# Kernel tuning notes

Hardware: AMD Instinct MI355X
Metric: run time of the kernel (lower is better)

The kernel has to match this reference:

```python
import jax, jax.numpy as jnp
import numpy as np

B, VD, SD, CD, H, HEADS = 16384, 2048, 1024, 512, 256, 4
DH = H // HEADS
EPS = 1e-5


def layer_norm(x, g, b):
    m = jnp.mean(x, axis=-1, keepdims=True)
    v = jnp.var(x, axis=-1, keepdims=True)
    return (x - m) * jax.lax.rsqrt(v + EPS) * g + b


def setup_inputs() -> dict:
    key = jax.random.key(0)
    ks = jax.random.split(key, 16)
    sc = 0.02
    inp = {
        'fv': jax.random.normal(ks[0], (B, VD), jnp.float32),
        'fs': jax.random.normal(ks[1], (B, SD), jnp.float32),
        'fc': jax.random.normal(ks[2], (B, CD), jnp.float32),
        # projection linears + layernorms
        'Wv': jax.random.normal(ks[3], (H, VD), jnp.float32) * sc,
        'bv': jnp.zeros((H,), jnp.float32),
        'gv': jnp.ones((H,), jnp.float32), 'bev': jnp.zeros((H,), jnp.float32),
        'Ws': jax.random.normal(ks[4], (H, SD), jnp.float32) * sc,
        'bs': jnp.zeros((H,), jnp.float32),
        'gs': jnp.ones((H,), jnp.float32), 'bes': jnp.zeros((H,), jnp.float32),
        'Wc': jax.random.normal(ks[5], (H, CD), jnp.float32) * sc,
        'bc': jnp.zeros((H,), jnp.float32),
        'gc_': jnp.ones((H,), jnp.float32), 'bec': jnp.zeros((H,), jnp.float32),
        # MultiheadAttention packed in-proj and out-proj
        'in_w': jax.random.normal(ks[6], (3 * H, H), jnp.float32) * sc,
        'in_b': jnp.zeros((3 * H,), jnp.float32),
        'out_w': jax.random.normal(ks[7], (H, H), jnp.float32) * sc,
        'out_b': jnp.zeros((H,), jnp.float32),
        # post-attention layernorm
        'gn': jnp.ones((H,), jnp.float32), 'gb': jnp.zeros((H,), jnp.float32),
        # gating MLP: Linear(3H,64) -> GELU -> Linear(64,3) -> softmax
        'g1w': jax.random.normal(ks[8], (64, 3 * H), jnp.float32) * sc,
        'g1b': jnp.zeros((64,), jnp.float32),
        'g2w': jax.random.normal(ks[9], (3, 64), jnp.float32) * sc,
        'g2b': jnp.zeros((3,), jnp.float32),
    }
    return inp


def reference(fv, fs, fc, Wv, bv, gv, bev, Ws, bs, gs, bes, Wc, bc, gc_, bec,
              in_w, in_b, out_w, out_b, gn, gb, g1w, g1b, g2w, g2b):
    v = layer_norm(fv @ Wv.T + bv, gv, bev)   # [B,H]
    s = layer_norm(fs @ Ws.T + bs, gs, bes)
    c = layer_norm(fc @ Wc.T + bc, gc_, bec)
    stack = jnp.stack([v, s, c], axis=1)      # [B,3,H]

    # self-attention over seq=3 (eval mode: dropout off)
    qkv = stack @ in_w.T + in_b               # [B,3,3H]
    q, k, vv = jnp.split(qkv, 3, axis=-1)
    def heads(x):  # [B,3,H] -> [B,HEADS,3,DH]
        return x.reshape(B, 3, HEADS, DH).transpose(0, 2, 1, 3)
    q, k, vv = heads(q), heads(k), heads(vv)
    scores = jnp.einsum('bhqd,bhkd->bhqk', q, k) / jnp.sqrt(jnp.float32(DH))
    attn = jax.nn.softmax(scores, axis=-1)
    ctx = jnp.einsum('bhqk,bhkd->bhqd', attn, vv)
    ctx = ctx.transpose(0, 2, 1, 3).reshape(B, 3, H)
    attended = ctx @ out_w.T + out_b          # [B,3,H]

    attended = layer_norm(attended + stack, gn, gb)
    av, as_, ac = attended[:, 0], attended[:, 1], attended[:, 2]

    h1 = jax.nn.gelu(jnp.concatenate([av, as_, ac], axis=-1) @ g1w.T + g1b, approximate=False)
    gates = jax.nn.softmax(h1 @ g2w.T + g2b, axis=-1)  # [B,3]

    fused = gates[:, 0:1] * av + gates[:, 1:2] * as_ + gates[:, 2:3] * ac
    return (fused, gates)
```

## Files before the change

kernel.cpp:

```cpp
#include <hip/hip_runtime.h>
#include <math.h>


typedef unsigned short u16;
typedef __bf16 bf16x8 __attribute__((ext_vector_type(8)));
typedef float fx4 __attribute__((ext_vector_type(4)));

#define MFMA_BF16(A_, B_, C_) __builtin_amdgcn_mfma_f32_16x16x32_bf16((A_), (B_), (C_), 0, 0, 0)

__device__ __forceinline__ float bf2f(u16 s) {
    union { float f; unsigned u; } c; c.u = ((unsigned)s) << 16; return c.f;
}
__device__ __forceinline__ u16 f2bf(float f) {
    union { float f; unsigned u; } c; c.f = f;
    return (u16)((c.u + 0x7fffu + ((c.u >> 16) & 1u)) >> 16);
}
__device__ __forceinline__ float bfpair_dot(unsigned a, unsigned b) {
    union { unsigned u; float f; } al, ah, bl, bh;
    al.u = a << 16; ah.u = a & 0xffff0000u;
    bl.u = b << 16; bh.u = b & 0xffff0000u;
    return al.f * bl.f + ah.f * bh.f;
}
__device__ __forceinline__ void gld16(void* l, const void* g) {
    __builtin_amdgcn_global_load_lds((const __attribute__((address_space(1))) void*)g,
                                     (__attribute__((address_space(3))) void*)l, 16, 0, 0);
}

__global__ __launch_bounds__(256) void cvt_w(const float* Wv, const float* Ws, const float* Wc,
                                             const float* inw, const float* outw, const float* g1w,
                                             u16* dst) {
    int idx = blockIdx.x * 256 + threadIdx.x;
    const float* src; int rel;
    if      (idx <  524288) { src = Wv;   rel = idx; }
    else if (idx <  786432) { src = Ws;   rel = idx -  524288; }
    else if (idx <  917504) { src = Wc;   rel = idx -  786432; }
    else if (idx < 1114112) { src = inw;  rel = idx -  917504; }
    else if (idx < 1179648) { src = outw; rel = idx - 1114112; }
    else                    { src = g1w;  rel = idx - 1179648; }
    dst[idx] = f2bf(src[rel]);
}

__global__ __launch_bounds__(256, 6) void gemm_ln(
    const float* fv, const float* fs, const float* fc,
    const u16* wWv, const u16* wWs, const u16* wWc,
    const float* bv, const float* gv, const float* bev,
    const float* bs, const float* gs, const float* bes,
    const float* bc, const float* gc_, const float* bec,
    u16* stack) {
    __shared__ alignas(16) char smem[20224];
    u16* sA = (u16*)smem;
    u16* sB = (u16*)(smem + 2560);
    u16* sC = (u16*)smem;
    float* redS = (float*)(smem + 18944);
    float* redQ = redS + 128;
    float* mvS  = redQ + 128;

    int bid = blockIdx.x;
    int slot, mblk;
    if (bid < 512)       { slot = 0; mblk = bid; }
    else if (bid < 1024) { slot = 1; mblk = bid - 512; }
    else                 { slot = 2; mblk = bid - 1024; }

    const float* A; const u16* W; const float* bias; const float* gg; const float* be; int K;
    if (slot == 0)      { A = fv; W = wWv; bias = bv; gg = gv;  be = bev; K = 2048; }
    else if (slot == 1) { A = fs; W = wWs; bias = bs; gg = gs;  be = bes; K = 1024; }
    else                { A = fc; W = wWc; bias = bc; gg = gc_; be = bec; K = 512;  }

    int t = threadIdx.x, wv = t >> 6, ln = t & 63, q = ln >> 4, l15 = ln & 15;
    int m0 = mblk * 32;

    fx4 zero = {0.f, 0.f, 0.f, 0.f};
    fx4 acc[2][4];
    #pragma unroll
    for (int mi = 0; mi < 2; ++mi)
        #pragma unroll
        for (int ni = 0; ni < 4; ++ni) acc[mi][ni] = zero;

    int rowA = t >> 3, ca = t & 7;
    const float* aBase = A + (size_t)(m0 + rowA) * K + ca * 4;
    u16* sAw = sA + rowA * 40 + ca * 4;

    int niter = K >> 5;
    for (int kt = 0; kt < niter; ++kt) {
        #pragma unroll
        for (int i = 0; i < 4; ++i) {
            int d = wv * 256 + i * 64 + ln;
            int n = d >> 2, p = d & 3;
            int kc = p ^ ((n >> 1) & 3);
            gld16((char*)sB + (wv * 256 + i * 64) * 16, W + (size_t)n * K + kt * 32 + kc * 8);
        }
        float4 f0 = *(const float4*)(aBase + kt * 32);
        union { u16 us[4]; uint2 v; } pk;
        pk.us[0] = f2bf(f0.x); pk.us[1] = f2bf(f0.y); pk.us[2] = f2bf(f0.z); pk.us[3] = f2bf(f0.w);
        *(uint2*)sAw = pk.v;
        __syncthreads();
        bf16x8 af[2], bfr[4];
        #pragma unroll
        for (int mi = 0; mi < 2; ++mi)
            af[mi] = *(const bf16x8*)(sA + (mi * 16 + l15) * 40 + q * 8);
        #pragma unroll
        for (int ni = 0; ni < 4; ++ni) {
            int n = wv * 64 + ni * 16 + l15;
            int ch = n * 4 + (q ^ ((n >> 1) & 3));
            bfr[ni] = *(const bf16x8*)(sB + ch * 8);
        }
        #pragma unroll
        for (int mi = 0; mi < 2; ++mi)
            #pragma unroll
            for (int ni = 0; ni < 4; ++ni)
                acc[mi][ni] = MFMA_BF16(af[mi], bfr[ni], acc[mi][ni]);
        __syncthreads();
    }

    float biasv[4], gvv[4], bevv[4];
    #pragma unroll
    for (int ni = 0; ni < 4; ++ni) {
        int col = wv * 64 + ni * 16 + l15;
        biasv[ni] = bias[col]; gvv[ni] = gg[col]; bevv[ni] = be[col];
    }
    #pragma unroll
    for (int mi = 0; mi < 2; ++mi)
        #pragma unroll
        for (int ni = 0; ni < 4; ++ni)
            #pragma unroll
            for (int r = 0; r < 4; ++r) acc[mi][ni][r] += biasv[ni];
    #pragma unroll
    for (int mi = 0; mi < 2; ++mi) {
        #pragma unroll
        for (int r = 0; r < 4; ++r) {
            float s = 0.f, qq = 0.f;
            #pragma unroll
            for (int ni = 0; ni < 4; ++ni) { float x = acc[mi][ni][r]; s += x; qq += x * x; }
            #pragma unroll
            for (int m = 1; m < 16; m <<= 1) { s += __shfl_xor(s, m, 64); qq += __shfl_xor(qq, m, 64); }
            if (l15 == 0) { int rho = mi * 16 + q * 4 + r; redS[rho * 4 + wv] = s; redQ[rho * 4 + wv] = qq; }
        }
    }
    __syncthreads();
    if (t < 32) {
        float s = redS[t * 4] + redS[t * 4 + 1] + redS[t * 4 + 2] + redS[t * 4 + 3];
        float qq = redQ[t * 4] + redQ[t * 4 + 1] + redQ[t * 4 + 2] + redQ[t * 4 + 3];
        float mean = s * (1.f / 256.f);
        float var = qq * (1.f / 256.f) - mean * mean;
        mvS[t * 2] = mean; mvS[t * 2 + 1] = rsqrtf(var + 1e-5f);
    }
    __syncthreads();
    #pragma unroll
    for (int mi = 0; mi < 2; ++mi) {
        #pragma unroll
        for (int r = 0; r < 4; ++r) {
            int rho = mi * 16 + q * 4 + r;
            float mean = mvS[rho * 2], rstd = mvS[rho * 2 + 1];
            #pragma unroll
            for (int ni = 0; ni < 4; ++ni) {
                int col = wv * 64 + ni * 16 + l15;
                float x = (acc[mi][ni][r] - mean) * rstd * gvv[ni] + bevv[ni];
                sC[rho * 256 + col] = f2bf(x);
            }
        }
    }
    __syncthreads();
    u16* outp = stack + (size_t)m0 * 768 + slot * 256;
    #pragma unroll
    for (int it = 0; it < 4; ++it) {
        int idx = t + it * 256;
        int row = idx >> 5, c = idx & 31;
        uint4 v = *(const uint4*)(sC + row * 256 + c * 8);
        *(uint4*)(outp + (size_t)row * 768 + c * 8) = v;
    }
}

__global__ __launch_bounds__(256) void gemm_qkv(const u16* stack, const u16* W, const float* in_b,
                                                u16* qkv) {
    __shared__ alignas(16) char smem[32768];
    u16* sA = (u16*)smem;
    u16* sB = (u16*)(smem + 8192);
    u16* sC = (u16*)smem;

    int t = threadIdx.x, wv = t >> 6, ln = t & 63, q = ln >> 4, l15 = ln & 15;
    int n0 = blockIdx.x * 128, m0 = blockIdx.y * 128;
    int wr = wv >> 1, wc = wv & 1;

    fx4 zero = {0.f, 0.f, 0.f, 0.f};
    fx4 acc[4][4];
    #pragma unroll
    for (int mi = 0; mi < 4; ++mi)
        #pragma unroll
        for (int ni = 0; ni < 4; ++ni) acc[mi][ni] = zero;

    for (int kt = 0; kt < 8; ++kt) {
        #pragma unroll
        for (int i = 0; i < 2; ++i) {
            int d = wv * 128 + i * 64 + ln;
            int r = d >> 2, p = d & 3;
            int kc = p ^ ((r >> 1) & 3);
            gld16((char*)sA + (wv * 128 + i * 64) * 16, stack + (size_t)(m0 + r) * 256 + kt * 32 + kc * 8);
            gld16((char*)sB + (wv * 128 + i * 64) * 16, W + (size_t)(n0 + r) * 256 + kt * 32 + kc * 8);
        }
        __syncthreads();
        bf16x8 af[4], bfr[4];
        #pragma unroll
        for (int mi = 0; mi < 4; ++mi) {
            int r = wr * 64 + mi * 16 + l15;
            int ch = r * 4 + (q ^ ((r >> 1) & 3));
            af[mi] = *(const bf16x8*)(sA + ch * 8);
        }
        #pragma unroll
        for (int ni = 0; ni < 4; ++ni) {
            int n = wc * 64 + ni * 16 + l15;
            int ch = n * 4 + (q ^ ((n >> 1) & 3));
            bfr[ni] = *(const bf16x8*)(sB + ch * 8);
        }
        #pragma unroll
        for (int mi = 0; mi < 4; ++mi)
            #pragma unroll
            for (int ni = 0; ni < 4; ++ni)
                acc[mi][ni] = MFMA_BF16(af[mi], bfr[ni], acc[mi][ni]);
        __syncthreads();
    }
    float biasv[4];
    #pragma unroll
    for (int ni = 0; ni < 4; ++ni) biasv[ni] = in_b[n0 + wc * 64 + ni * 16 + l15];
    #pragma unroll
    for (int mi = 0; mi < 4; ++mi)
        #pragma unroll
        for (int ni = 0; ni < 4; ++ni)
            #pragma unroll
            for (int r = 0; r < 4; ++r) {
                int rl = wr * 64 + mi * 16 + q * 4 + r;
                int cl = wc * 64 + ni * 16 + l15;
                sC[rl * 128 + cl] = f2bf(acc[mi][ni][r] + biasv[ni]);
            }
    __syncthreads();
    #pragma unroll
    for (int it = 0; it < 8; ++it) {
        int idx = t + it * 256;
        int row = idx >> 4, c = idx & 15;
        uint4 v = *(const uint4*)(sC + row * 128 + c * 8);
        *(uint4*)(qkv + (size_t)(m0 + row) * 768 + n0 + c * 8) = v;
    }
}

__global__ __launch_bounds__(256) void attn_k(const u16* qkv, u16* ctx) {
    __shared__ alignas(16) char smem[38016];
    u16* qs = (u16*)smem;
    float* sS = (float*)(smem + 36864);

    int t = threadIdx.x, wv = t >> 6, ln = t & 63;
    size_t base = (size_t)blockIdx.x * 8 * 2304;
    #pragma unroll
    for (int i = 0; i < 9; ++i) {
        int d = wv * 576 + i * 64;
        gld16((char*)smem + (size_t)d * 16, qkv + base + (size_t)(d + ln) * 8);
    }
    __syncthreads();
    #pragma unroll
    for (int it = 0; it < 2; ++it) {
        int idx = t + it * 256;
        if (idx < 288) {
            int b = idx / 36, rem = idx % 36, h = rem / 9, pp = rem % 9, i = pp / 3, j = pp % 3;
            const u16* qp = qs + b * 2304 + i * 768 + h * 64;
            const u16* kp = qs + b * 2304 + j * 768 + 256 + h * 64;
            float acc = 0.f;
            #pragma unroll
            for (int c = 0; c < 8; ++c) {
                uint4 qa = *(const uint4*)(qp + c * 8);
                uint4 ka = *(const uint4*)(kp + c * 8);
                acc += bfpair_dot(qa.x, ka.x) + bfpair_dot(qa.y, ka.y) +
                       bfpair_dot(qa.z, ka.z) + bfpair_dot(qa.w, ka.w);
            }
            sS[idx] = acc * 0.125f;
        }
    }
    __syncthreads();
    if (t < 96) {
        int b3 = t * 3;
        float s0 = sS[b3], s1 = sS[b3 + 1], s2 = sS[b3 + 2];
        float m = fmaxf(s0, fmaxf(s1, s2));
        float e0 = __expf(s0 - m), e1 = __expf(s1 - m), e2 = __expf(s2 - m);
        float inv = 1.f / (e0 + e1 + e2);
        sS[b3] = e0 * inv; sS[b3 + 1] = e1 * inv; sS[b3 + 2] = e2 * inv;
    }
    __syncthreads();
    #pragma unroll
    for (int it = 0; it < 3; ++it) {
        int idx = t + it * 256;
        int b = idx / 96, rem = idx % 96, i = rem / 32, c = rem & 31, h = c >> 3;
        int pbase = b * 36 + h * 9 + i * 3;
        float o[8];
        #pragma unroll
        for (int e = 0; e < 8; ++e) o[e] = 0.f;
        #pragma unroll
        for (int j = 0; j < 3; ++j) {
            float p = sS[pbase + j];
            uint4 va = *(const uint4*)(qs + b * 2304 + j * 768 + 512 + c * 8);
            unsigned uu[4] = {va.x, va.y, va.z, va.w};
            #pragma unroll
            for (int pr = 0; pr < 4; ++pr) {
                union { unsigned u; float f; } lo, hi;
                lo.u = uu[pr] << 16; hi.u = uu[pr] & 0xffff0000u;
                o[2 * pr]     += p * lo.f;
                o[2 * pr + 1] += p * hi.f;
            }
        }
        union { u16 us[8]; uint4 v; } pk;
        #pragma unroll
        for (int e = 0; e < 8; ++e) pk.us[e] = f2bf(o[e]);
        *(uint4*)(ctx + (size_t)(blockIdx.x * 8 + b) * 768 + i * 256 + c * 8) = pk.v;
    }
}

__global__ __launch_bounds__(256) void outproj_k(
    const u16* ctx, const u16* W, const float* out_b, const u16* stack,
    const float* gn, const float* gb, const u16* g1w, const float* g1b,
    const float* g2w, const float* g2b, float* outF, float* outG) {
    __shared__ alignas(16) char smem[40960];
    u16* r1 = (u16*)smem;
    u16* sB = (u16*)(smem + 24576);
    float* redS = (float*)(smem + 24576);
    float* redQ = redS + 192;
    float* mvS = redQ + 192;
    float* h1S = (float*)(smem + 26624);
    float* lgS = (float*)(smem + 30720);
    float* gateS = lgS + 48;

    int t = threadIdx.x, wv = t >> 6, ln = t & 63, q = ln >> 4, l15 = ln & 15;
    int gr0 = blockIdx.x * 48, b0 = blockIdx.x * 16;

    #pragma unroll
    for (int i = 0; i < 6; ++i) {
        int d = wv * 384 + i * 64 + ln;
        int row = d >> 5, p = d & 31;
        int kc = p ^ (row & 7);
        gld16((char*)r1 + (wv * 384 + i * 64) * 16, ctx + (size_t)(gr0 + row) * 256 + kc * 8);
    }
    __syncthreads();

    fx4 zero = {0.f, 0.f, 0.f, 0.f};
    fx4 acc[3][4];
    #pragma unroll
    for (int mi = 0; mi < 3; ++mi)
        #pragma unroll
        for (int ni = 0; ni < 4; ++ni) acc[mi][ni] = zero;

    for (int kt = 0; kt < 8; ++kt) {
        #pragma unroll
        for (int i = 0; i < 4; ++i) {
            int d = wv * 256 + i * 64 + ln;
            int n = d >> 2, p = d & 3;
            int kc = p ^ ((n >> 1) & 3);
            gld16((char*)sB + (wv * 256 + i * 64) * 16, W + (size_t)n * 256 + kt * 32 + kc * 8);
        }
        __syncthreads();
        bf16x8 af[3], bfr[4];
        #pragma unroll
        for (int mi = 0; mi < 3; ++mi) {
            int row = mi * 16 + l15;
            int ch = row * 32 + ((kt * 4 + q) ^ (row & 7));
            af[mi] = *(const bf16x8*)(r1 + ch * 8);
        }
        #pragma unroll
        for (int ni = 0; ni < 4; ++ni) {
            int n = wv * 64 + ni * 16 + l15;
            int ch = n * 4 + (q ^ ((n >> 1) & 3));
            bfr[ni] = *(const bf16x8*)(sB + ch * 8);
        }
        #pragma unroll
        for (int mi = 0; mi < 3; ++mi)
            #pragma unroll
            for (int ni = 0; ni < 4; ++ni)
                acc[mi][ni] = MFMA_BF16(af[mi], bfr[ni], acc[mi][ni]);
        __syncthreads();
    }

    #pragma unroll
    for (int i = 0; i < 6; ++i) {
        int d = wv * 384 + i * 64 + ln;
        gld16((char*)r1 + (wv * 384 + i * 64) * 16, stack + (size_t)gr0 * 256 + (size_t)d * 8);
    }
    __syncthreads();

    float obv[4], gnv[4], gbv[4];
    #pragma unroll
    for (int ni = 0; ni < 4; ++ni) {
        int col = wv * 64 + ni * 16 + l15;
        obv[ni] = out_b[col]; gnv[ni] = gn[col]; gbv[ni] = gb[col];
    }
    #pragma unroll
    for (int mi = 0; mi < 3; ++mi)
        #pragma unroll
        for (int ni = 0; ni < 4; ++ni)
            #pragma unroll
            for (int r = 0; r < 4; ++r) {
                int rho = mi * 16 + q * 4 + r;
                int col = wv * 64 + ni * 16 + l15;
                acc[mi][ni][r] += obv[ni] + bf2f(r1[rho * 256 + col]);
            }
    #pragma unroll
    for (int mi = 0; mi < 3; ++mi) {
        #pragma unroll
        for (int r = 0; r < 4; ++r) {
            float s = 0.f, qq = 0.f;
            #pragma unroll
            for (int ni = 0; ni < 4; ++ni) { float x = acc[mi][ni][r]; s += x; qq += x * x; }
            #pragma unroll
            for (int m = 1; m < 16; m <<= 1) { s += __shfl_xor(s, m, 64); qq += __shfl_xor(qq, m, 64); }
            if (l15 == 0) { int rho = mi * 16 + q * 4 + r; redS[rho * 4 + wv] = s; redQ[rho * 4 + wv] = qq; }
        }
    }
    __syncthreads();
    if (t < 48) {
        float s = redS[t * 4] + redS[t * 4 + 1] + redS[t * 4 + 2] + redS[t * 4 + 3];
        float qq = redQ[t * 4] + redQ[t * 4 + 1] + redQ[t * 4 + 2] + redQ[t * 4 + 3];
        float mean = s * (1.f / 256.f);
        float var = qq * (1.f / 256.f) - mean * mean;
        mvS[t * 2] = mean; mvS[t * 2 + 1] = rsqrtf(var + 1e-5f);
    }
    __syncthreads();
    #pragma unroll
    for (int mi = 0; mi < 3; ++mi) {
        #pragma unroll
        for (int r = 0; r < 4; ++r) {
            int rho = mi * 16 + q * 4 + r;
            float mean = mvS[rho * 2], rstd = mvS[rho * 2 + 1];
            int bl = rho / 3, sl = rho - bl * 3;
            #pragma unroll
            for (int ni = 0; ni < 4; ++ni) {
                int col = wv * 64 + ni * 16 + l15;
                float x = (acc[mi][ni][r] - mean) * rstd * gnv[ni] + gbv[ni];
                int k = sl * 256 + col;
                int kidx = k >> 3, wn = k & 7;
                r1[(bl * 96 + (kidx ^ (bl & 7))) * 8 + wn] = f2bf(x);
            }
        }
    }
    __syncthreads();
    fx4 ag = zero;
    for (int kt = 0; kt < 24; ++kt) {
        int bl = l15;
        int kidx = kt * 4 + q;
        bf16x8 afr = *(const bf16x8*)(r1 + (bl * 96 + (kidx ^ (bl & 7))) * 8);
        int n = wv * 16 + l15;
        bf16x8 bfr2 = *(const bf16x8*)(g1w + (size_t)n * 768 + kt * 32 + q * 8);
        ag = MFMA_BF16(afr, bfr2, ag);
    }
    #pragma unroll
    for (int r = 0; r < 4; ++r) {
        int bl = q * 4 + r, n = wv * 16 + l15;
        float x = ag[r] + g1b[n];
        h1S[bl * 64 + n] = 0.5f * x * (1.f + erff(x * 0.70710678118f));
    }
    __syncthreads();
    if (t < 48) {
        int bl = t / 3, s = t - bl * 3;
        float a = g2b[s];
        #pragma unroll
        for (int k = 0; k < 64; ++k) a += h1S[bl * 64 + k] * g2w[s * 64 + k];
        lgS[t] = a;
    }
    __syncthreads();
    if (t < 48) {
        int bl = t / 3, s = t - bl * 3;
        float l0 = lgS[bl * 3], l1 = lgS[bl * 3 + 1], l2 = lgS[bl * 3 + 2];
        float m = fmaxf(l0, fmaxf(l1, l2));
        float e0 = __expf(l0 - m), e1 = __expf(l1 - m), e2 = __expf(l2 - m);
        float inv = 1.f / (e0 + e1 + e2);
        float gsel = ((s == 0) ? e0 : (s == 1) ? e1 : e2) * inv;
        gateS[t] = gsel;
        outG[(size_t)(b0 + bl) * 3 + s] = gsel;
    }
    __syncthreads();
    #pragma unroll
    for (int it = 0; it < 2; ++it) {
        int idx = t + it * 256;
        int b = idx >> 5, c = idx & 31;
        float g0 = gateS[b * 3], g1 = gateS[b * 3 + 1], g2 = gateS[b * 3 + 2];
        float o[8];
        #pragma unroll
        for (int e = 0; e < 8; ++e) o[e] = 0.f;
        #pragma unroll
        for (int s = 0; s < 3; ++s) {
            float gw = (s == 0) ? g0 : (s == 1) ? g1 : g2;
            int kidx = s * 32 + c;
            uint4 raw = *(const uint4*)(r1 + (b * 96 + (kidx ^ (b & 7))) * 8);
            unsigned uu[4] = {raw.x, raw.y, raw.z, raw.w};
            #pragma unroll
            for (int pr = 0; pr < 4; ++pr) {
                union { unsigned u; float f; } lo, hi;
                lo.u = uu[pr] << 16; hi.u = uu[pr] & 0xffff0000u;
                o[2 * pr]     += gw * lo.f;
                o[2 * pr + 1] += gw * hi.f;
            }
        }
        float* op = outF + (size_t)(b0 + b) * 256 + c * 8;
        float4 v0; v0.x = o[0]; v0.y = o[1]; v0.z = o[2]; v0.w = o[3];
        float4 v1; v1.x = o[4]; v1.y = o[5]; v1.z = o[6]; v1.w = o[7];
        *(float4*)op = v0;
        *(float4*)(op + 4) = v1;
    }
}

extern "C" void kernel_launch(void* const* d_in, const int* in_sizes, int n_in,
                              void* d_out, int out_size, void* d_ws, size_t ws_size,
                              hipStream_t stream) {
    (void)in_sizes; (void)n_in; (void)out_size; (void)ws_size;
    const float* fv   = (const float*)d_in[0];
    const float* fs   = (const float*)d_in[1];
    const float* fc   = (const float*)d_in[2];
    const float* Wv   = (const float*)d_in[3];
    const float* bv   = (const float*)d_in[4];
    const float* gv   = (const float*)d_in[5];
    const float* bev  = (const float*)d_in[6];
    const float* Ws   = (const float*)d_in[7];
    const float* bs   = (const float*)d_in[8];
    const float* gs   = (const float*)d_in[9];
    const float* bes  = (const float*)d_in[10];
    const float* Wc   = (const float*)d_in[11];
    const float* bc   = (const float*)d_in[12];
    const float* gc_  = (const float*)d_in[13];
    const float* bec  = (const float*)d_in[14];
    const float* in_w = (const float*)d_in[15];
    const float* in_b = (const float*)d_in[16];
    const float* out_w= (const float*)d_in[17];
    const float* out_b= (const float*)d_in[18];
    const float* gn   = (const float*)d_in[19];
    const float* gb   = (const float*)d_in[20];
    const float* g1w  = (const float*)d_in[21];
    const float* g1b  = (const float*)d_in[22];
    const float* g2w  = (const float*)d_in[23];
    const float* g2b  = (const float*)d_in[24];

    u16* w0    = (u16*)d_ws;
    u16* wWv   = w0;
    u16* wWs   = w0 + 524288;
    u16* wWc   = w0 + 786432;
    u16* wIn   = w0 + 917504;
    u16* wOut  = w0 + 1114112;
    u16* wG1   = w0 + 1179648;
    u16* stack = w0 + 1228800;
    u16* qkv   = w0 + 13811712;
    u16* ctx   = w0 + 51560448;
    float* outF = (float*)d_out;
    float* outG = outF + (size_t)16384 * 256;

    cvt_w<<<4800, 256, 0, stream>>>(Wv, Ws, Wc, in_w, out_w, g1w, w0);
    gemm_ln<<<1536, 256, 0, stream>>>(fv, fs, fc, wWv, wWs, wWc,
                                      bv, gv, bev, bs, gs, bes, bc, gc_, bec, stack);
    gemm_qkv<<<dim3(6, 384), 256, 0, stream>>>(stack, wIn, in_b, qkv);
    attn_k<<<2048, 256, 0, stream>>>(qkv, ctx);
    outproj_k<<<1024, 256, 0, stream>>>(ctx, wOut, out_b, stack, gn, gb,
                                        wG1, g1b, g2w, g2b, outF, outG);
}
```

Before: 477.1 us.

## Enlarge GEMM tiles in projection and QKV kernels to reuse weight tiles

Result: faster. 463.8 us (-2.8%).

```diff
diff --git a/kernel.cpp b/kernel.cpp
--- a/kernel.cpp
+++ b/kernel.cpp
@@ -40,26 +40,26 @@
     dst[idx] = f2bf(src[rel]);
 }
 
-__global__ __launch_bounds__(256, 6) void gemm_ln(
+__global__ __launch_bounds__(256, 2) void gemm_ln(
     const float* fv, const float* fs, const float* fc,
     const u16* wWv, const u16* wWs, const u16* wWc,
     const float* bv, const float* gv, const float* bev,
     const float* bs, const float* gs, const float* bes,
     const float* bc, const float* gc_, const float* bec,
     u16* stack) {
-    __shared__ alignas(16) char smem[20224];
+    __shared__ alignas(16) char smem[70656];
     u16* sA = (u16*)smem;
-    u16* sB = (u16*)(smem + 2560);
+    u16* sB = (u16*)(smem + 10240);
     u16* sC = (u16*)smem;
-    float* redS = (float*)(smem + 18944);
-    float* redQ = redS + 128;
-    float* mvS  = redQ + 128;
+    float* redS = (float*)(smem + 65536);
+    float* redQ = (float*)(smem + 67584);
+    float* mvS  = (float*)(smem + 69632);
 
     int bid = blockIdx.x;
     int slot, mblk;
-    if (bid < 512)       { slot = 0; mblk = bid; }
-    else if (bid < 1024) { slot = 1; mblk = bid - 512; }
-    else                 { slot = 2; mblk = bid - 1024; }
+    if (bid < 128)      { slot = 0; mblk = bid; }
+    else if (bid < 256) { slot = 1; mblk = bid - 128; }
+    else                { slot = 2; mblk = bid - 256; }
 
     const float* A; const u16* W; const float* bias; const float* gg; const float* be; int K;
     if (slot == 0)      { A = fv; W = wWv; bias = bv; gg = gv;  be = bev; K = 2048; }
@@ -67,36 +67,47 @@
     else                { A = fc; W = wWc; bias = bc; gg = gc_; be = bec; K = 512;  }
 
     int t = threadIdx.x, wv = t >> 6, ln = t & 63, q = ln >> 4, l15 = ln & 15;
-    int m0 = mblk * 32;
+    int m0 = mblk * 128;
 
     fx4 zero = {0.f, 0.f, 0.f, 0.f};
-    fx4 acc[2][4];
-    #pragma unroll
-    for (int mi = 0; mi < 2; ++mi)
+    fx4 acc[8][4];
+    #pragma unroll
+    for (int mi = 0; mi < 8; ++mi)
         #pragma unroll
         for (int ni = 0; ni < 4; ++ni) acc[mi][ni] = zero;
 
-    int rowA = t >> 3, ca = t & 7;
-    const float* aBase = A + (size_t)(m0 + rowA) * K + ca * 4;
-    u16* sAw = sA + rowA * 40 + ca * 4;
+    int rowA = t >> 1, ca = t & 1;
+    const float* aBase = A + (size_t)(m0 + rowA) * K + ca * 16;
+    u16* sAw = sA + rowA * 40 + ca * 16;
+
+    int bN[4], bKc[4];
+    #pragma unroll
+    for (int i = 0; i < 4; ++i) {
+        int d = wv * 256 + i * 64 + ln;
+        bN[i] = d >> 2;
+        bKc[i] = (d & 3) ^ ((bN[i] >> 1) & 3);
+    }
 
     int niter = K >> 5;
     for (int kt = 0; kt < niter; ++kt) {
         #pragma unroll
-        for (int i = 0; i < 4; ++i) {
-            int d = wv * 256 + i * 64 + ln;
-            int n = d >> 2, p = d & 3;
-            int kc = p ^ ((n >> 1) & 3);
-            gld16((char*)sB + (wv * 256 + i * 64) * 16, W + (size_t)n * K + kt * 32 + kc * 8);
-        }
+        for (int i = 0; i < 4; ++i)
+            gld16((char*)sB + (wv * 256 + i * 64) * 16, W + (size_t)bN[i] * K + kt * 32 + bKc[i] * 8);
         float4 f0 = *(const float4*)(aBase + kt * 32);
-        union { u16 us[4]; uint2 v; } pk;
-        pk.us[0] = f2bf(f0.x); pk.us[1] = f2bf(f0.y); pk.us[2] = f2bf(f0.z); pk.us[3] = f2bf(f0.w);
-        *(uint2*)sAw = pk.v;
+        float4 f1 = *(const float4*)(aBase + kt * 32 + 4);
+        float4 f2 = *(const float4*)(aBase + kt * 32 + 8);
+        float4 f3 = *(const float4*)(aBase + kt * 32 + 12);
+        union { u16 us[8]; uint4 v; } p0, p1;
+        p0.us[0] = f2bf(f0.x); p0.us[1] = f2bf(f0.y); p0.us[2] = f2bf(f0.z); p0.us[3] = f2bf(f0.w);
+        p0.us[4] = f2bf(f1.x); p0.us[5] = f2bf(f1.y); p0.us[6] = f2bf(f1.z); p0.us[7] = f2bf(f1.w);
+        p1.us[0] = f2bf(f2.x); p1.us[1] = f2bf(f2.y); p1.us[2] = f2bf(f2.z); p1.us[3] = f2bf(f2.w);
+        p1.us[4] = f2bf(f3.x); p1.us[5] = f2bf(f3.y); p1.us[6] = f2bf(f3.z); p1.us[7] = f2bf(f3.w);
+        *(uint4*)sAw = p0.v;
+        *(uint4*)(sAw + 8) = p1.v;
         __syncthreads();
-        bf16x8 af[2], bfr[4];
-        #pragma unroll
-        for (int mi = 0; mi < 2; ++mi)
+        bf16x8 af[8], bfr[4];
+        #pragma unroll
+        for (int mi = 0; mi < 8; ++mi)
             af[mi] = *(const bf16x8*)(sA + (mi * 16 + l15) * 40 + q * 8);
         #pragma unroll
         for (int ni = 0; ni < 4; ++ni) {
@@ -105,7 +116,7 @@
             bfr[ni] = *(const bf16x8*)(sB + ch * 8);
         }
         #pragma unroll
-        for (int mi = 0; mi < 2; ++mi)
+        for (int mi = 0; mi < 8; ++mi)
             #pragma unroll
             for (int ni = 0; ni < 4; ++ni)
                 acc[mi][ni] = MFMA_BF16(af[mi], bfr[ni], acc[mi][ni]);
@@ -119,13 +130,13 @@
         biasv[ni] = bias[col]; gvv[ni] = gg[col]; bevv[ni] = be[col];
     }
     #pragma unroll
-    for (int mi = 0; mi < 2; ++mi)
+    for (int mi = 0; mi < 8; ++mi)
         #pragma unroll
         for (int ni = 0; ni < 4; ++ni)
             #pragma unroll
             for (int r = 0; r < 4; ++r) acc[mi][ni][r] += biasv[ni];
     #pragma unroll
-    for (int mi = 0; mi < 2; ++mi) {
+    for (int mi = 0; mi < 8; ++mi) {
         #pragma unroll
         for (int r = 0; r < 4; ++r) {
             float s = 0.f, qq = 0.f;
@@ -137,7 +148,7 @@
         }
     }
     __syncthreads();
-    if (t < 32) {
+    if (t < 128) {
         float s = redS[t * 4] + redS[t * 4 + 1] + redS[t * 4 + 2] + redS[t * 4 + 3];
         float qq = redQ[t * 4] + redQ[t * 4 + 1] + redQ[t * 4 + 2] + redQ[t * 4 + 3];
         float mean = s * (1.f / 256.f);
@@ -146,7 +157,7 @@
     }
     __syncthreads();
     #pragma unroll
-    for (int mi = 0; mi < 2; ++mi) {
+    for (int mi = 0; mi < 8; ++mi) {
         #pragma unroll
         for (int r = 0; r < 4; ++r) {
             int rho = mi * 16 + q * 4 + r;
@@ -162,7 +173,7 @@
     __syncthreads();
     u16* outp = stack + (size_t)m0 * 768 + slot * 256;
     #pragma unroll
-    for (int it = 0; it < 4; ++it) {
+    for (int it = 0; it < 16; ++it) {
         int idx = t + it * 256;
         int row = idx >> 5, c = idx & 31;
         uint4 v = *(const uint4*)(sC + row * 256 + c * 8);
@@ -170,35 +181,50 @@
     }
 }
 
-__global__ __launch_bounds__(256) void gemm_qkv(const u16* stack, const u16* W, const float* in_b,
-                                                u16* qkv) {
-    __shared__ alignas(16) char smem[32768];
+__global__ __launch_bounds__(256, 2) void gemm_qkv(const u16* stack, const u16* W, const float* in_b,
+                                                   u16* qkv) {
+    __shared__ alignas(16) char smem[65536];
     u16* sA = (u16*)smem;
     u16* sB = (u16*)(smem + 8192);
     u16* sC = (u16*)smem;
 
     int t = threadIdx.x, wv = t >> 6, ln = t & 63, q = ln >> 4, l15 = ln & 15;
-    int n0 = blockIdx.x * 128, m0 = blockIdx.y * 128;
+    int n0 = blockIdx.x * 256, m0 = blockIdx.y * 128;
     int wr = wv >> 1, wc = wv & 1;
 
     fx4 zero = {0.f, 0.f, 0.f, 0.f};
-    fx4 acc[4][4];
+    fx4 acc[4][8];
     #pragma unroll
     for (int mi = 0; mi < 4; ++mi)
         #pragma unroll
-        for (int ni = 0; ni < 4; ++ni) acc[mi][ni] = zero;
+        for (int ni = 0; ni < 8; ++ni) acc[mi][ni] = zero;
+
+    int aR[2], aKc[2];
+    #pragma unroll
+    for (int i = 0; i < 2; ++i) {
+        int d = wv * 128 + i * 64 + ln;
+        aR[i] = d >> 2;
+        aKc[i] = (d & 3) ^ ((aR[i] >> 1) & 3);
+    }
+    int bN[4], bKc[4];
+    #pragma unroll
+    for (int i = 0; i < 4; ++i) {
+        int d = wv * 256 + i * 64 + ln;
+        bN[i] = d >> 2;
+        bKc[i] = (d & 3) ^ ((bN[i] >> 1) & 3);
+    }
 
     for (int kt = 0; kt < 8; ++kt) {
         #pragma unroll
-        for (int i = 0; i < 2; ++i) {
-            int d = wv * 128 + i * 64 + ln;
-            int r = d >> 2, p = d & 3;
-            int kc = p ^ ((r >> 1) & 3);
-            gld16((char*)sA + (wv * 128 + i * 64) * 16, stack + (size_t)(m0 + r) * 256 + kt * 32 + kc * 8);
-            gld16((char*)sB + (wv * 128 + i * 64) * 16, W + (size_t)(n0 + r) * 256 + kt * 32 + kc * 8);
-        }
+        for (int i = 0; i < 2; ++i)
+            gld16((char*)sA + (wv * 128 + i * 64) * 16,
+                  stack + (size_t)(m0 + aR[i]) * 256 + kt * 32 + aKc[i] * 8);
+        #pragma unroll
+        for (int i = 0; i < 4; ++i)
+            gld16((char*)sB + (wv * 256 + i * 64) * 16,
+                  W + (size_t)(n0 + bN[i]) * 256 + kt * 32 + bKc[i] * 8);
         __syncthreads();
-        bf16x8 af[4], bfr[4];
+        bf16x8 af[4], bfr[8];
         #pragma unroll
         for (int mi = 0; mi < 4; ++mi) {
             int r = wr * 64 + mi * 16 + l15;
@@ -206,37 +232,38 @@
             af[mi] = *(const bf16x8*)(sA + ch * 8);
         }
         #pragma unroll
-        for (int ni = 0; ni < 4; ++ni) {
-            int n = wc * 64 + ni * 16 + l15;
+        for (int ni = 0; ni < 8; ++ni) {
+            int n = wc * 128 + ni * 16 + l15;
             int ch = n * 4 + (q ^ ((n >> 1) & 3));
             bfr[ni] = *(const bf16x8*)(sB + ch * 8);
         }
         #pragma unroll
         for (int mi = 0; mi < 4; ++mi)
             #pragma unroll
-            for (int ni = 0; ni < 4; ++ni)
+            for (int ni = 0; ni < 8; ++ni)
                 acc[mi][ni] = MFMA_BF16(af[mi], bfr[ni], acc[mi][ni]);
         __syncthreads();
     }
-    float biasv[4];
-    #pragma unroll
-    for (int ni = 0; ni < 4; ++ni) biasv[ni] = in_b[n0 + wc * 64 + ni * 16 + l15];
+
+    float biasv[8];
+    #pragma unroll
+    for (int ni = 0; ni < 8; ++ni) biasv[ni] = in_b[n0 + wc * 128 + ni * 16 + l15];
     #pragma unroll
     for (int mi = 0; mi < 4; ++mi)
         #pragma unroll
-        for (int ni = 0; ni < 4; ++ni)
+        for (int ni = 0; ni < 8; ++ni)
             #pragma unroll
             for (int r = 0; r < 4; ++r) {
                 int rl = wr * 64 + mi * 16 + q * 4 + r;
-                int cl = wc * 64 + ni * 16 + l15;
-                sC[rl * 128 + cl] = f2bf(acc[mi][ni][r] + biasv[ni]);
-            }
-    __syncthreads();
-    #pragma unroll
-    for (int it = 0; it < 8; ++it) {
+                int cl = wc * 128 + ni * 16 + l15;
+                sC[rl * 256 + cl] = f2bf(acc[mi][ni][r] + biasv[ni]);
+            }
+    __syncthreads();
+    #pragma unroll
+    for (int it = 0; it < 16; ++it) {
         int idx = t + it * 256;
-        int row = idx >> 4, c = idx & 15;
-        uint4 v = *(const uint4*)(sC + row * 128 + c * 8);
+        int row = idx >> 5, c = idx & 31;
+        uint4 v = *(const uint4*)(sC + row * 256 + c * 8);
         *(uint4*)(qkv + (size_t)(m0 + row) * 768 + n0 + c * 8) = v;
     }
 }
@@ -544,9 +571,9 @@
     float* outG = outF + (size_t)16384 * 256;
 
     cvt_w<<<4800, 256, 0, stream>>>(Wv, Ws, Wc, in_w, out_w, g1w, w0);
-    gemm_ln<<<1536, 256, 0, stream>>>(fv, fs, fc, wWv, wWs, wWc,
-                                      bv, gv, bev, bs, gs, bes, bc, gc_, bec, stack);
-    gemm_qkv<<<dim3(6, 384), 256, 0, stream>>>(stack, wIn, in_b, qkv);
+    gemm_ln<<<384, 256, 0, stream>>>(fv, fs, fc, wWv, wWs, wWc,
+                                     bv, gv, bev, bs, gs, bes, bc, gc_, bec, stack);
+    gemm_qkv<<<dim3(3, 384), 256, 0, stream>>>(stack, wIn, in_b, qkv);
     attn_k<<<2048, 256, 0, stream>>>(qkv, ctx);
     outproj_k<<<1024, 256, 0, stream>>>(ctx, wOut, out_b, stack, gn, gb,
                                         wG1, g1b, g2w, g2b, outF, outG);
```
